# Kernel optimization log

Hardware: AMD Instinct MI355X
Metric: run time of the kernel (lower is better)

## Reference

```python
import jax, jax.numpy as jnp
import numpy as np

BATCH, FEAT, NUM, K = 8, 512, 512, 32

def _l2norm(v, axis):
    # matches F.normalize(p=2): v / max(||v||, eps)
    n = jnp.sqrt(jnp.sum(v * v, axis=axis, keepdims=True))
    return v / jnp.maximum(n, 1e-12)

def setup_inputs() -> dict:
    key = jax.random.key(0)
    k1, k2, k3, k4 = jax.random.split(key, 4)
    x = jax.random.normal(k1, (BATCH, FEAT, NUM), dtype=jnp.float32)
    W = jax.random.normal(k2, (K, FEAT), dtype=jnp.float32) * 0.02
    b = jnp.zeros((K,), dtype=jnp.float32)
    mu = jax.random.uniform(k3, (FEAT, K), dtype=jnp.float32)
    # sigma drawn away from 0 to keep the 1/sigma division well-conditioned
    sigma = jax.random.uniform(k4, (FEAT, K), dtype=jnp.float32, minval=0.5, maxval=1.0)
    return {"x": x, "W": W, "b": b, "mu": mu, "sigma": sigma}

def reference(x, W, b, mu, sigma):
    batch, feat, num = x.shape
    xt = jnp.transpose(x, (0, 2, 1))                      # [b, n, f]
    a = jax.nn.softmax(xt @ W.T + b, axis=2)              # [b, n, k]
    # Fused reduction over n: f = (x - mu)/sigma, fv1 = sum_n a*f, fv2 = sum_n a*(f^2-1)
    asum = jnp.sum(a, axis=1)                             # [b, k]
    ax = jnp.einsum('bnk,bnf->bfk', a, xt)                # sum_n a * x
    ax2 = jnp.einsum('bnk,bnf->bfk', a, xt * xt)          # sum_n a * x^2
    mu_b = mu[None]                                       # [1, f, k]
    sig_b = sigma[None]
    asum_b = asum[:, None, :]                             # [b, 1, k]
    fv1 = (ax - mu_b * asum_b) / sig_b                    # [b, f, k]
    fv2 = (ax2 - 2.0 * mu_b * ax + mu_b * mu_b * asum_b) / (sig_b * sig_b) - asum_b
    fv1 = _l2norm(fv1, 2).reshape(batch, -1)
    fv1 = _l2norm(fv1, 1)
    fv2 = _l2norm(fv2, 2).reshape(batch, -1)
    fv2 = _l2norm(fv2, 1)
    return jnp.concatenate([fv1, fv2], axis=1)            # [b, 2*f*k]
```

## Files before the change

kernel.cpp:

```cpp
#include <hip/hip_runtime.h>


#define B_ 8
#define F_ 512
#define N_ 512
#define K_ 32

__global__ __launch_bounds__(256) void k_a(const float* __restrict__ x,
                                           const float* __restrict__ W,
                                           const float* __restrict__ bias,
                                           float* __restrict__ aP,
                                           float* __restrict__ asumP) {
  __shared__ float xs[128][18];
  __shared__ float ws[128][36];
  __shared__ float red[512][9];
  __shared__ float rmax[16], rinv[16];
  const int t  = threadIdx.x;
  const int b  = blockIdx.x >> 5;
  const int nt = blockIdx.x & 31;
  const int n0 = nt << 4;
  const int fs = t >> 5;
  const int kg = (t >> 2) & 7;
  const int ng = t & 3;
  const int n4 = ng * 4, k4 = kg * 4;

  float acc[4][4] = {{0.f}};

  for (int ph = 0; ph < 4; ++ph) {
    const int fb = ph << 7;
#pragma unroll
    for (int it = 0; it < 8; ++it) {
      int flat = t + 256 * it;
      int f = flat >> 4, nn = flat & 15;
      xs[f][nn] = x[(size_t)(b * F_ + fb + f) * N_ + n0 + nn];
    }
#pragma unroll
    for (int it = 0; it < 16; ++it) {
      int flat = t + 256 * it;
      int k = flat >> 7, f = flat & 127;
      ws[f][k] = W[k * F_ + fb + f];
    }
    __syncthreads();
    const int fBeg = fs << 4;
#pragma unroll
    for (int fi = 0; fi < 16; ++fi) {
      const int f = fBeg + fi;
      const float2 x01 = *(const float2*)&xs[f][n4];
      const float2 x23 = *(const float2*)&xs[f][n4 + 2];
      const float4 wv  = *(const float4*)&ws[f][k4];
      acc[0][0] += x01.x * wv.x; acc[0][1] += x01.x * wv.y;
      acc[0][2] += x01.x * wv.z; acc[0][3] += x01.x * wv.w;
      acc[1][0] += x01.y * wv.x; acc[1][1] += x01.y * wv.y;
      acc[1][2] += x01.y * wv.z; acc[1][3] += x01.y * wv.w;
      acc[2][0] += x23.x * wv.x; acc[2][1] += x23.x * wv.y;
      acc[2][2] += x23.x * wv.z; acc[2][3] += x23.x * wv.w;
      acc[3][0] += x23.y * wv.x; acc[3][1] += x23.y * wv.y;
      acc[3][2] += x23.y * wv.z; acc[3][3] += x23.y * wv.w;
    }
    __syncthreads();
  }

#pragma unroll
  for (int i = 0; i < 4; ++i)
#pragma unroll
    for (int j = 0; j < 4; ++j)
      red[(n4 + i) * 32 + k4 + j][fs] = acc[i][j];
  __syncthreads();

  const int o0 = 2 * t, o1 = 2 * t + 1;
  float l0 = bias[o0 & 31], l1 = bias[o1 & 31];
#pragma unroll
  for (int s = 0; s < 8; ++s) { l0 += red[o0][s]; l1 += red[o1][s]; }
  red[o0][8] = l0;
  red[o1][8] = l1;
  __syncthreads();

  if (t < 16) {
    float m = -1e30f;
#pragma unroll
    for (int j = 0; j < 32; ++j) m = fmaxf(m, red[t * 32 + j][8]);
    float ssum = 0.f;
#pragma unroll
    for (int j = 0; j < 32; ++j) ssum += __expf(red[t * 32 + j][8] - m);
    rmax[t] = m;
    rinv[t] = 1.f / ssum;
  }
  __syncthreads();

  const int row = o0 >> 5;
  const float m = rmax[row], inv = rinv[row];
  const float a0 = __expf(l0 - m) * inv;
  const float a1 = __expf(l1 - m) * inv;
  float2 av; av.x = a0; av.y = a1;
  *(float2*)&aP[(size_t)(b * N_ + n0 + row) * K_ + (o0 & 31)] = av;

  red[o0][8] = a0;
  red[o1][8] = a1;
  __syncthreads();
  if (t < 32) {
    float s = 0.f;
#pragma unroll
    for (int nl = 0; nl < 16; ++nl) s += red[nl * 32 + t][8];
    asumP[(b * 32 + nt) * 32 + t] = s;
  }
}

__global__ __launch_bounds__(256) void k_ax(const float* __restrict__ x,
                                            const float* __restrict__ aP,
                                            float* __restrict__ axP,
                                            float* __restrict__ ax2P) {
  __shared__ float xsT[64][132];
  __shared__ float as_[64][36];
  const int t  = threadIdx.x;
  const int s  = blockIdx.x & 7;
  const int ft = (blockIdx.x >> 3) & 3;
  const int b  = blockIdx.x >> 5;
  const int f0 = ft << 7;
  const int n0 = s << 6;
  const int fg = t >> 3, kg = t & 7;
  const int f4 = fg * 4, k4 = kg * 4;

#pragma unroll
  for (int it = 0; it < 32; ++it) {
    int flat = t + 256 * it;
    int r = flat >> 6, nn = flat & 63;
    xsT[nn][r] = x[(size_t)(b * F_ + f0 + r) * N_ + n0 + nn];
  }
#pragma unroll
  for (int it = 0; it < 8; ++it) {
    int flat = t + 256 * it;
    int r = flat >> 5, kk = flat & 31;
    as_[r][kk] = aP[(size_t)(b * N_ + n0 + r) * K_ + kk];
  }
  __syncthreads();

  float ax[4][4] = {{0.f}}, bx[4][4] = {{0.f}};
#pragma unroll 4
  for (int n = 0; n < 64; ++n) {
    const float4 xv = *(const float4*)&xsT[n][f4];
    const float4 av = *(const float4*)&as_[n][k4];
    const float* xp = &xv.x;
    const float* ap = &av.x;
#pragma unroll
    for (int i = 0; i < 4; ++i) {
      const float xi = xp[i];
      const float xq = xi * xi;
#pragma unroll
      for (int j = 0; j < 4; ++j) {
        ax[i][j] += xi * ap[j];
        bx[i][j] += xq * ap[j];
      }
    }
  }

  const size_t base = ((size_t)(s * B_ + b) * F_ + f0 + f4) * K_ + k4;
#pragma unroll
  for (int i = 0; i < 4; ++i) {
    float4 v1, v2;
    v1.x = ax[i][0]; v1.y = ax[i][1]; v1.z = ax[i][2]; v1.w = ax[i][3];
    v2.x = bx[i][0]; v2.y = bx[i][1]; v2.z = bx[i][2]; v2.w = bx[i][3];
    *(float4*)&axP [base + (size_t)i * K_] = v1;
    *(float4*)&ax2P[base + (size_t)i * K_] = v2;
  }
}

__global__ __launch_bounds__(256) void k_fv(const float* __restrict__ axP,
                                            const float* __restrict__ ax2P,
                                            const float* __restrict__ asumP,
                                            const float* __restrict__ mu,
                                            const float* __restrict__ sg,
                                            float* __restrict__ out) {
  __shared__ float sm[32];
  const int t = threadIdx.x;
  const int g = blockIdx.x * 256 + t;
  const int k = g & 31;
  const int f = (g >> 5) & (F_ - 1);
  const int b = g >> 14;

  if (t < 32) {
    float s = 0.f;
#pragma unroll
    for (int nt = 0; nt < 32; ++nt) s += asumP[(b * 32 + nt) * 32 + t];
    sm[t] = s;
  }
  __syncthreads();

  float ax = 0.f, ax2 = 0.f;
#pragma unroll
  for (int s = 0; s < 8; ++s) {
    ax  += axP [(size_t)((s * B_ + b) * F_ + f) * K_ + k];
    ax2 += ax2P[(size_t)((s * B_ + b) * F_ + f) * K_ + k];
  }
  const float m  = mu[f * K_ + k];
  const float sd = sg[f * K_ + k];
  const float as = sm[k];

  const float fv1 = (ax - m * as) / sd;
  const float fv2 = (ax2 - 2.f * m * ax + m * m * as) / (sd * sd) - as;

  float s1 = fv1 * fv1, s2 = fv2 * fv2;
#pragma unroll
  for (int off = 16; off >= 1; off >>= 1) {
    s1 += __shfl_xor(s1, off, 32);
    s2 += __shfl_xor(s2, off, 32);
  }
  const float inv512 = 0.04419417382415922f;
  const float o1 = fv1 / fmaxf(sqrtf(s1), 1e-12f) * inv512;
  const float o2 = fv2 / fmaxf(sqrtf(s2), 1e-12f) * inv512;

  out[(size_t)b * (2 * F_ * K_) + f * K_ + k] = o1;
  out[(size_t)b * (2 * F_ * K_) + F_ * K_ + f * K_ + k] = o2;
}

extern "C" void kernel_launch(void* const* d_in, const int* in_sizes, int n_in,
                              void* d_out, int out_size, void* d_ws, size_t ws_size,
                              hipStream_t stream) {
  const float* x  = (const float*)d_in[0];
  const float* W  = (const float*)d_in[1];
  const float* bv = (const float*)d_in[2];
  const float* mu = (const float*)d_in[3];
  const float* sg = (const float*)d_in[4];
  float* out = (float*)d_out;

  float* ws    = (float*)d_ws;
  float* aP    = ws;
  float* axP   = ws + 131072;
  float* ax2P  = ws + 131072 + 1048576;
  float* asumP = ws + 131072 + 2 * 1048576;

  hipLaunchKernelGGL(k_a,  dim3(256), dim3(256), 0, stream, x, W, bv, aP, asumP);
  hipLaunchKernelGGL(k_ax, dim3(256), dim3(256), 0, stream, x, aP, axP, ax2P);
  hipLaunchKernelGGL(k_fv, dim3(512), dim3(256), 0, stream, axP, ax2P, asumP, mu, sg, out);
}
```

Baseline: 86.39 us.

## Fuse ax and fv kernels via atomic counter barrier, double-buffer and swizzle k_a

Merges the partial-sum kernel and the normalization kernel into one launch. Each group of 8 split-n blocks signals an atomic counter and spin-waits until its siblings finish, then reduces the partials and writes the normalized output. The first kernel now prefetches the next x/W tile into registers while computing on the current one. It also uses XOR-swizzled shared layouts, an 8-wide k tile per thread, and shuffle-based softmax and asum reductions. This removes one launch and some LDS bank conflicts, but the spin-wait depends on all 256 blocks being resident at the same time, which could deadlock otherwise.

```diff
diff --git a/kernel.cpp b/kernel.cpp
--- a/kernel.cpp
+++ b/kernel.cpp
@@ -10,107 +10,167 @@
                                            const float* __restrict__ W,
                                            const float* __restrict__ bias,
                                            float* __restrict__ aP,
-                                           float* __restrict__ asumP) {
+                                           float* __restrict__ asumP,
+                                           unsigned int* __restrict__ ctr) {
   __shared__ float xs[128][18];
-  __shared__ float ws[128][36];
-  __shared__ float red[512][9];
-  __shared__ float rmax[16], rinv[16];
-  const int t  = threadIdx.x;
+  __shared__ float ws[128 * 32];
+  __shared__ float red2[16][516];
+  __shared__ float sm4[4][32];
+  const int t = threadIdx.x;
+  if (blockIdx.x == 0 && t < 32) ctr[t] = 0u;
+
   const int b  = blockIdx.x >> 5;
   const int nt = blockIdx.x & 31;
   const int n0 = nt << 4;
-  const int fs = t >> 5;
-  const int kg = (t >> 2) & 7;
   const int ng = t & 3;
-  const int n4 = ng * 4, k4 = kg * 4;
-
-  float acc[4][4] = {{0.f}};
+  const int kg = (t >> 2) & 3;
+  const int fs = t >> 4;
+  const int n4 = ng * 4;
+  const int k8 = kg * 8;
+
+  float acc[4][8];
+#pragma unroll
+  for (int i = 0; i < 4; ++i)
+#pragma unroll
+    for (int j = 0; j < 8; ++j) acc[i][j] = 0.f;
+
+  float xr[8], wr[16];
+#pragma unroll
+  for (int it = 0; it < 8; ++it) {
+    int flat = t + 256 * it;
+    xr[it] = x[(size_t)(b * F_ + (flat >> 4)) * N_ + n0 + (flat & 15)];
+  }
+#pragma unroll
+  for (int it = 0; it < 16; ++it) {
+    int flat = t + 256 * it;
+    wr[it] = W[(flat >> 7) * F_ + (flat & 127)];
+  }
+#pragma unroll
+  for (int it = 0; it < 8; ++it) {
+    int flat = t + 256 * it;
+    xs[flat >> 4][flat & 15] = xr[it];
+  }
+#pragma unroll
+  for (int it = 0; it < 16; ++it) {
+    int flat = t + 256 * it;
+    int f = flat & 127, k = flat >> 7;
+    ws[f * 32 + (k ^ (f & 31))] = wr[it];
+  }
+  __syncthreads();
 
   for (int ph = 0; ph < 4; ++ph) {
-    const int fb = ph << 7;
-#pragma unroll
-    for (int it = 0; it < 8; ++it) {
-      int flat = t + 256 * it;
-      int f = flat >> 4, nn = flat & 15;
-      xs[f][nn] = x[(size_t)(b * F_ + fb + f) * N_ + n0 + nn];
-    }
-#pragma unroll
-    for (int it = 0; it < 16; ++it) {
-      int flat = t + 256 * it;
-      int k = flat >> 7, f = flat & 127;
-      ws[f][k] = W[k * F_ + fb + f];
-    }
-    __syncthreads();
-    const int fBeg = fs << 4;
-#pragma unroll
-    for (int fi = 0; fi < 16; ++fi) {
-      const int f = fBeg + fi;
+    if (ph < 3) {
+      const int fb = (ph + 1) << 7;
+#pragma unroll
+      for (int it = 0; it < 8; ++it) {
+        int flat = t + 256 * it;
+        xr[it] = x[(size_t)(b * F_ + fb + (flat >> 4)) * N_ + n0 + (flat & 15)];
+      }
+#pragma unroll
+      for (int it = 0; it < 16; ++it) {
+        int flat = t + 256 * it;
+        wr[it] = W[(flat >> 7) * F_ + fb + (flat & 127)];
+      }
+    }
+#pragma unroll
+    for (int fi = 0; fi < 8; ++fi) {
+      const int f = fs * 8 + fi;
       const float2 x01 = *(const float2*)&xs[f][n4];
       const float2 x23 = *(const float2*)&xs[f][n4 + 2];
-      const float4 wv  = *(const float4*)&ws[f][k4];
-      acc[0][0] += x01.x * wv.x; acc[0][1] += x01.x * wv.y;
-      acc[0][2] += x01.x * wv.z; acc[0][3] += x01.x * wv.w;
-      acc[1][0] += x01.y * wv.x; acc[1][1] += x01.y * wv.y;
-      acc[1][2] += x01.y * wv.z; acc[1][3] += x01.y * wv.w;
-      acc[2][0] += x23.x * wv.x; acc[2][1] += x23.x * wv.y;
-      acc[2][2] += x23.x * wv.z; acc[2][3] += x23.x * wv.w;
-      acc[3][0] += x23.y * wv.x; acc[3][1] += x23.y * wv.y;
-      acc[3][2] += x23.y * wv.z; acc[3][3] += x23.y * wv.w;
+      const float4 wA = *(const float4*)&ws[f * 32 + ((k8) ^ (f & 28))];
+      const float4 wB = *(const float4*)&ws[f * 32 + ((k8 + 4) ^ (f & 28))];
+      const float xv[4] = {x01.x, x01.y, x23.x, x23.y};
+      const float wa[4] = {((const float*)&wA)[0 ^ (fi & 3)],
+                           ((const float*)&wA)[1 ^ (fi & 3)],
+                           ((const float*)&wA)[2 ^ (fi & 3)],
+                           ((const float*)&wA)[3 ^ (fi & 3)]};
+      const float wb[4] = {((const float*)&wB)[0 ^ (fi & 3)],
+                           ((const float*)&wB)[1 ^ (fi & 3)],
+                           ((const float*)&wB)[2 ^ (fi & 3)],
+                           ((const float*)&wB)[3 ^ (fi & 3)]};
+#pragma unroll
+      for (int i = 0; i < 4; ++i)
+#pragma unroll
+        for (int j = 0; j < 4; ++j) {
+          acc[i][j]     += xv[i] * wa[j];
+          acc[i][4 + j] += xv[i] * wb[j];
+        }
     }
     __syncthreads();
-  }
-
-#pragma unroll
-  for (int i = 0; i < 4; ++i)
-#pragma unroll
-    for (int j = 0; j < 4; ++j)
-      red[(n4 + i) * 32 + k4 + j][fs] = acc[i][j];
-  __syncthreads();
-
-  const int o0 = 2 * t, o1 = 2 * t + 1;
-  float l0 = bias[o0 & 31], l1 = bias[o1 & 31];
-#pragma unroll
-  for (int s = 0; s < 8; ++s) { l0 += red[o0][s]; l1 += red[o1][s]; }
-  red[o0][8] = l0;
-  red[o1][8] = l1;
-  __syncthreads();
-
-  if (t < 16) {
-    float m = -1e30f;
-#pragma unroll
-    for (int j = 0; j < 32; ++j) m = fmaxf(m, red[t * 32 + j][8]);
-    float ssum = 0.f;
-#pragma unroll
-    for (int j = 0; j < 32; ++j) ssum += __expf(red[t * 32 + j][8] - m);
-    rmax[t] = m;
-    rinv[t] = 1.f / ssum;
-  }
-  __syncthreads();
-
-  const int row = o0 >> 5;
-  const float m = rmax[row], inv = rinv[row];
-  const float a0 = __expf(l0 - m) * inv;
-  const float a1 = __expf(l1 - m) * inv;
+    if (ph < 3) {
+#pragma unroll
+      for (int it = 0; it < 8; ++it) {
+        int flat = t + 256 * it;
+        xs[flat >> 4][flat & 15] = xr[it];
+      }
+#pragma unroll
+      for (int it = 0; it < 16; ++it) {
+        int flat = t + 256 * it;
+        int f = flat & 127, k = flat >> 7;
+        ws[f * 32 + (k ^ (f & 31))] = wr[it];
+      }
+      __syncthreads();
+    }
+  }
+
+#pragma unroll
+  for (int i = 0; i < 4; ++i) {
+    float4 v1, v2;
+    v1.x = acc[i][0]; v1.y = acc[i][1]; v1.z = acc[i][2]; v1.w = acc[i][3];
+    v2.x = acc[i][4]; v2.y = acc[i][5]; v2.z = acc[i][6]; v2.w = acc[i][7];
+    *(float4*)&red2[fs][(n4 + i) * 32 + k8] = v1;
+    *(float4*)&red2[fs][(n4 + i) * 32 + k8 + 4] = v2;
+  }
+  __syncthreads();
+
+  const int o0 = 2 * t;
+  const int row = t >> 4;
+  const int k0 = o0 & 31;
+  float l0 = bias[k0], l1 = bias[k0 + 1];
+#pragma unroll
+  for (int s2 = 0; s2 < 16; ++s2) {
+    float2 r = *(const float2*)&red2[s2][o0];
+    l0 += r.x; l1 += r.y;
+  }
+  float m = fmaxf(l0, l1);
+  m = fmaxf(m, __shfl_xor(m, 1));
+  m = fmaxf(m, __shfl_xor(m, 2));
+  m = fmaxf(m, __shfl_xor(m, 4));
+  m = fmaxf(m, __shfl_xor(m, 8));
+  const float e0 = __expf(l0 - m), e1 = __expf(l1 - m);
+  float ssum = e0 + e1;
+  ssum += __shfl_xor(ssum, 1);
+  ssum += __shfl_xor(ssum, 2);
+  ssum += __shfl_xor(ssum, 4);
+  ssum += __shfl_xor(ssum, 8);
+  const float inv = 1.f / ssum;
+  const float a0 = e0 * inv, a1 = e1 * inv;
   float2 av; av.x = a0; av.y = a1;
-  *(float2*)&aP[(size_t)(b * N_ + n0 + row) * K_ + (o0 & 31)] = av;
-
-  red[o0][8] = a0;
-  red[o1][8] = a1;
+  *(float2*)&aP[(size_t)(b * N_ + n0 + row) * K_ + k0] = av;
+
+  float s0 = a0 + __shfl_xor(a0, 16); s0 += __shfl_xor(s0, 32);
+  float s1 = a1 + __shfl_xor(a1, 16); s1 += __shfl_xor(s1, 32);
+  const int l = t & 63, w = t >> 6;
+  if (l < 16) { sm4[w][2 * l] = s0; sm4[w][2 * l + 1] = s1; }
   __syncthreads();
   if (t < 32) {
-    float s = 0.f;
-#pragma unroll
-    for (int nl = 0; nl < 16; ++nl) s += red[nl * 32 + t][8];
-    asumP[(b * 32 + nt) * 32 + t] = s;
+    float tot = sm4[0][t] + sm4[1][t] + sm4[2][t] + sm4[3][t];
+    asumP[(b * 32 + nt) * 32 + t] = tot;
   }
 }
 
-__global__ __launch_bounds__(256) void k_ax(const float* __restrict__ x,
-                                            const float* __restrict__ aP,
-                                            float* __restrict__ axP,
-                                            float* __restrict__ ax2P) {
-  __shared__ float xsT[64][132];
+__global__ __launch_bounds__(256) void k_ax_fv(const float* __restrict__ x,
+                                               const float* __restrict__ aP,
+                                               const float* __restrict__ asumP,
+                                               const float* __restrict__ mu,
+                                               const float* __restrict__ sg,
+                                               float* __restrict__ axP,
+                                               float* __restrict__ ax2P,
+                                               unsigned int* __restrict__ ctr,
+                                               float* __restrict__ out) {
+  __shared__ float xsT[64 * 128];
   __shared__ float as_[64][36];
+  __shared__ float sm[32];
   const int t  = threadIdx.x;
   const int s  = blockIdx.x & 7;
   const int ft = (blockIdx.x >> 3) & 3;
@@ -123,8 +183,9 @@
 #pragma unroll
   for (int it = 0; it < 32; ++it) {
     int flat = t + 256 * it;
-    int r = flat >> 6, nn = flat & 63;
-    xsT[nn][r] = x[(size_t)(b * F_ + f0 + r) * N_ + n0 + nn];
+    int f = flat >> 6, nn = flat & 63;
+    xsT[nn * 128 + (f ^ (nn & 31))] =
+        x[(size_t)(b * F_ + f0 + f) * N_ + n0 + nn];
   }
 #pragma unroll
   for (int it = 0; it < 8; ++it) {
@@ -135,81 +196,86 @@
   __syncthreads();
 
   float ax[4][4] = {{0.f}}, bx[4][4] = {{0.f}};
-#pragma unroll 4
-  for (int n = 0; n < 64; ++n) {
-    const float4 xv = *(const float4*)&xsT[n][f4];
-    const float4 av = *(const float4*)&as_[n][k4];
-    const float* xp = &xv.x;
-    const float* ap = &av.x;
-#pragma unroll
-    for (int i = 0; i < 4; ++i) {
-      const float xi = xp[i];
-      const float xq = xi * xi;
-#pragma unroll
-      for (int j = 0; j < 4; ++j) {
-        ax[i][j] += xi * ap[j];
-        bx[i][j] += xq * ap[j];
-      }
-    }
-  }
-
-  const size_t base = ((size_t)(s * B_ + b) * F_ + f0 + f4) * K_ + k4;
+#pragma unroll 2
+  for (int nb = 0; nb < 64; nb += 4) {
+#pragma unroll
+    for (int u = 0; u < 4; ++u) {
+      const int n = nb + u;
+      const float4 xv = *(const float4*)&xsT[n * 128 + (f4 ^ (n & 28))];
+      const float4 av = *(const float4*)&as_[n][k4];
+      const float* xp = (const float*)&xv;
+      const float* ap = (const float*)&av;
+#pragma unroll
+      for (int i = 0; i < 4; ++i) {
+        const float xi = xp[i ^ u];
+        const float xq = xi * xi;
+#pragma unroll
+        for (int j = 0; j < 4; ++j) {
+          ax[i][j] += xi * ap[j];
+          bx[i][j] += xq * ap[j];
+        }
+      }
+    }
+  }
+
+  const size_t pbase = ((size_t)(s * B_ + b) * F_ + f0 + f4) * K_ + k4;
 #pragma unroll
   for (int i = 0; i < 4; ++i) {
     float4 v1, v2;
     v1.x = ax[i][0]; v1.y = ax[i][1]; v1.z = ax[i][2]; v1.w = ax[i][3];
     v2.x = bx[i][0]; v2.y = bx[i][1]; v2.z = bx[i][2]; v2.w = bx[i][3];
-    *(float4*)&axP [base + (size_t)i * K_] = v1;
-    *(float4*)&ax2P[base + (size_t)i * K_] = v2;
-  }
-}
-
-__global__ __launch_bounds__(256) void k_fv(const float* __restrict__ axP,
-                                            const float* __restrict__ ax2P,
-                                            const float* __restrict__ asumP,
-                                            const float* __restrict__ mu,
-                                            const float* __restrict__ sg,
-                                            float* __restrict__ out) {
-  __shared__ float sm[32];
-  const int t = threadIdx.x;
-  const int g = blockIdx.x * 256 + t;
-  const int k = g & 31;
-  const int f = (g >> 5) & (F_ - 1);
-  const int b = g >> 14;
+    *(float4*)&axP [pbase + (size_t)i * K_] = v1;
+    *(float4*)&ax2P[pbase + (size_t)i * K_] = v2;
+  }
+
+  __threadfence();
+  __syncthreads();
+  if (t == 0) {
+    unsigned int* c = &ctr[b * 4 + ft];
+    atomicAdd(c, 1u);
+    while (__hip_atomic_load(c, __ATOMIC_ACQUIRE, __HIP_MEMORY_SCOPE_AGENT) < 8u)
+      __builtin_amdgcn_s_sleep(2);
+  }
+  __syncthreads();
+  __threadfence();
 
   if (t < 32) {
-    float s = 0.f;
-#pragma unroll
-    for (int nt = 0; nt < 32; ++nt) s += asumP[(b * 32 + nt) * 32 + t];
-    sm[t] = s;
-  }
-  __syncthreads();
-
-  float ax = 0.f, ax2 = 0.f;
-#pragma unroll
-  for (int s = 0; s < 8; ++s) {
-    ax  += axP [(size_t)((s * B_ + b) * F_ + f) * K_ + k];
-    ax2 += ax2P[(size_t)((s * B_ + b) * F_ + f) * K_ + k];
-  }
-  const float m  = mu[f * K_ + k];
-  const float sd = sg[f * K_ + k];
-  const float as = sm[k];
-
-  const float fv1 = (ax - m * as) / sd;
-  const float fv2 = (ax2 - 2.f * m * ax + m * m * as) / (sd * sd) - as;
-
-  float s1 = fv1 * fv1, s2 = fv2 * fv2;
-#pragma unroll
-  for (int off = 16; off >= 1; off >>= 1) {
-    s1 += __shfl_xor(s1, off, 32);
-    s2 += __shfl_xor(s2, off, 32);
-  }
-  const float inv512 = 0.04419417382415922f;
-  const float o1 = fv1 / fmaxf(sqrtf(s1), 1e-12f) * inv512;
-  const float o2 = fv2 / fmaxf(sqrtf(s2), 1e-12f) * inv512;
-
-  out[(size_t)b * (2 * F_ * K_) + f * K_ + k] = o1;
-  out[(size_t)b * (2 * F_ * K_) + F_ * K_ + f * K_ + k] = o2;
+    float tot = 0.f;
+#pragma unroll
+    for (int nt = 0; nt < 32; ++nt) tot += asumP[(b * 32 + nt) * 32 + t];
+    sm[t] = tot;
+  }
+  __syncthreads();
+
+  const int k  = t & 31;
+  const int fl = t >> 5;
+#pragma unroll
+  for (int c = 0; c < 2; ++c) {
+    const int f = f0 + s * 16 + c * 8 + fl;
+    float axv = 0.f, ax2v = 0.f;
+#pragma unroll
+    for (int sl = 0; sl < 8; ++sl) {
+      const size_t idx = ((size_t)(sl * B_ + b) * F_ + f) * K_ + k;
+      axv  += axP[idx];
+      ax2v += ax2P[idx];
+    }
+    const float m  = mu[f * K_ + k];
+    const float sd = sg[f * K_ + k];
+    const float as = sm[k];
+    const float fv1 = (axv - m * as) / sd;
+    const float fv2 = (ax2v - 2.f * m * axv + m * m * as) / (sd * sd) - as;
+    float s1 = fv1 * fv1, s2 = fv2 * fv2;
+#pragma unroll
+    for (int off = 16; off >= 1; off >>= 1) {
+      s1 += __shfl_xor(s1, off);
+      s2 += __shfl_xor(s2, off);
+    }
+    const float inv512 = 0.04419417382415922f;
+    out[(size_t)b * 32768 + f * 32 + k] =
+        fv1 / fmaxf(sqrtf(s1), 1e-12f) * inv512;
+    out[(size_t)b * 32768 + 16384 + f * 32 + k] =
+        fv2 / fmaxf(sqrtf(s2), 1e-12f) * inv512;
+  }
 }
 
 extern "C" void kernel_launch(void* const* d_in, const int* in_sizes, int n_in,
@@ -227,8 +293,10 @@
   float* axP   = ws + 131072;
   float* ax2P  = ws + 131072 + 1048576;
   float* asumP = ws + 131072 + 2 * 1048576;
-
-  hipLaunchKernelGGL(k_a,  dim3(256), dim3(256), 0, stream, x, W, bv, aP, asumP);
-  hipLaunchKernelGGL(k_ax, dim3(256), dim3(256), 0, stream, x, aP, axP, ax2P);
-  hipLaunchKernelGGL(k_fv, dim3(512), dim3(256), 0, stream, axP, ax2P, asumP, mu, sg, out);
+  unsigned int* ctr = (unsigned int*)(asumP + 8192);
+
+  hipLaunchKernelGGL(k_a, dim3(256), dim3(256), 0, stream,
+                     x, W, bv, aP, asumP, ctr);
+  hipLaunchKernelGGL(k_ax_fv, dim3(256), dim3(256), 0, stream,
+                     x, aP, asumP, mu, sg, axP, ax2P, ctr, out);
 }
```

Result: slower. 142.4 us (+64.9%).
